# Kernel optimization log

Measured on AMD Instinct MI355X. Metric: run time of the kernel, lower is better.

Reference implementation:

```python
import jax, jax.numpy as jnp
import numpy as np

B, S, D, H = 2, 2048, 1024, 16
HD = D // H  # head_dim = 64
ROPE_BASE = 10000.0
NEG = -1e9


def rope_cos_sin(seq_len, head_dim, dtype):
    inv_freq = 1.0 / (ROPE_BASE ** (jnp.arange(0, head_dim, 2, dtype=jnp.float32) / head_dim))
    t = jnp.arange(seq_len, dtype=jnp.float32)
    freqs = jnp.outer(t, inv_freq)              # [S, HD/2]
    emb = jnp.concatenate([freqs, freqs], axis=-1)  # [S, HD]
    return jnp.cos(emb).astype(dtype), jnp.sin(emb).astype(dtype)


def rotate_half(x):
    half = x.shape[-1] // 2
    return jnp.concatenate([-x[..., half:], x[..., :half]], axis=-1)


def setup_inputs() -> dict:
    key = jax.random.key(0)
    ks = jax.random.split(key, 9)
    s = 0.02
    x = jax.random.normal(ks[0], (B, S, D), dtype=jnp.float32)
    # additive causal mask: 0 on/below diagonal, -1e9 above
    mask = jnp.where(jnp.tril(jnp.ones((S, S), dtype=bool)), 0.0, NEG).astype(jnp.float32)
    params = {
        'Wq': jax.random.normal(ks[1], (D, D), jnp.float32) * s,
        'bq': jnp.zeros((D,), jnp.float32),
        'Wk': jax.random.normal(ks[2], (D, D), jnp.float32) * s,
        'bk': jnp.zeros((D,), jnp.float32),
        'Wv': jax.random.normal(ks[3], (D, D), jnp.float32) * s,
        'bv': jnp.zeros((D,), jnp.float32),
        'Wo': jax.random.normal(ks[4], (D, D), jnp.float32) * s,
        'bo': jnp.zeros((D,), jnp.float32),
    }
    return {'x': x, 'mask': mask, **params}


def reference(x, mask, Wq, bq, Wk, bk, Wv, bv, Wo, bo):
    Bv, Sv, Dv = x.shape
    q = (x @ Wq + bq).reshape(Bv, Sv, H, HD).transpose(0, 2, 1, 3)  # [B,H,S,HD]
    k = (x @ Wk + bk).reshape(Bv, Sv, H, HD).transpose(0, 2, 1, 3)
    v = (x @ Wv + bv).reshape(Bv, Sv, H, HD).transpose(0, 2, 1, 3)
    cos, sin = rope_cos_sin(Sv, HD, x.dtype)      # [S, HD]
    cos = cos[None, None]                          # [1,1,S,HD]
    sin = sin[None, None]
    q = q * cos + rotate_half(q) * sin
    k = k * cos + rotate_half(k) * sin
    scale = jnp.asarray(np.sqrt(HD), x.dtype)
    scores = jnp.einsum('bhqd,bhkd->bhqk', q, k) / scale  # [B,H,S,S]
    scores = scores + mask[None, None]
    attn = jax.nn.softmax(scores, axis=-1)
    out = jnp.einsum('bhqk,bhkd->bhqd', attn, v)   # [B,H,S,HD]
    out = out.transpose(0, 2, 1, 3).reshape(Bv, Sv, Dv)
    return out @ Wo + bo
```

## Files before the change

### kernel.cpp

```cpp
#include <hip/hip_runtime.h>
#include <hip/hip_bf16.h>
#include <cstdint>

typedef __bf16 bf16;
typedef __bf16 bf16x4 __attribute__((ext_vector_type(4)));
typedef __bf16 bf16x8 __attribute__((ext_vector_type(8)));
typedef float f32x4 __attribute__((ext_vector_type(4)));

#define DEV __device__ __forceinline__

DEV void gl_lds16(const void* g, void* l) {
    __builtin_amdgcn_global_load_lds(
        (__attribute__((address_space(1))) void*)(uintptr_t)g,
        (__attribute__((address_space(3))) void*)(uint32_t)(uintptr_t)l,
        16, 0, 0);
}

DEV f32x4 mfma16(bf16x8 a, bf16x8 b, f32x4 c) {
    return __builtin_amdgcn_mfma_f32_16x16x32_bf16(a, b, c, 0, 0, 0);
}

__global__ __launch_bounds__(256) void prep_k(
    const float* __restrict__ x, bf16* __restrict__ xb,
    const float* __restrict__ w0, const float* __restrict__ w1,
    const float* __restrict__ w2, const float* __restrict__ w3,
    bf16* __restrict__ WT, float* __restrict__ cosT, float* __restrict__ sinT) {
    __shared__ float t[32][33];
    const int blk = (int)blockIdx.x;
    const int tid = threadIdx.x;
    if (blk < 4096) {
        const int i = blk * 256 + tid;
        const float4 v = ((const float4*)x)[i];
        bf16x4 o = {(bf16)v.x, (bf16)v.y, (bf16)v.z, (bf16)v.w};
        *(bf16x4*)(xb + (size_t)i * 4) = o;
    } else if (blk < 8192) {
        const int j = blk - 4096;
        const int z = j >> 10, jy = (j >> 5) & 31, jx = j & 31;
        const float* W = z == 0 ? w0 : z == 1 ? w1 : z == 2 ? w2 : w3;
        bf16* dst = WT + (size_t)z * 1024 * 1024;
        const int tx = tid & 31, ty = tid >> 5;
        const int kb = jx * 32, nb = jy * 32;
#pragma unroll
        for (int i = 0; i < 4; ++i)
            t[ty + i * 8][tx] = W[(size_t)(kb + ty + i * 8) * 1024 + nb + tx];
        __syncthreads();
#pragma unroll
        for (int i = 0; i < 4; ++i)
            dst[(size_t)(nb + ty + i * 8) * 1024 + kb + tx] = (bf16)t[tx][ty + i * 8];
    } else {
        const int tt = (blk - 8192) * 256 + tid;
        const int s = tt >> 6, i = tt & 31;
        const float inv = expf(-(float)i * (9.210340371976184f / 32.0f));
        const float ang = (float)s * inv;
        cosT[tt] = cosf(ang);
        sinT[tt] = sinf(ang);
    }
}

__global__ __launch_bounds__(512, 1) void gemm256_k(
    const bf16* __restrict__ A, const bf16* __restrict__ BT,
    const float* __restrict__ bq, const float* __restrict__ bk,
    const float* __restrict__ bv,
    bf16* __restrict__ outQ, bf16* __restrict__ outK, bf16* __restrict__ outV,
    const float* __restrict__ cosT, const float* __restrict__ sinT) {
    extern __shared__ char smem[];
    const int tid = threadIdx.x;
    const int lane = tid & 63, wv = tid >> 6;
    const int wm2 = wv >> 2, wn2 = wv & 3;
    const int q = lane & 15, g = lane >> 4;

    const int gid = (int)blockIdx.x;
    const int xcd = gid & 7, idx = gid >> 3;
    const int bm = (xcd & 3) * 4 + (idx & 3);
    const int bn = (xcd >> 2) * 6 + (idx >> 2);

    const bf16* Ab = A + (size_t)bm * 256 * 1024;
    const bf16* Bb = BT + (size_t)bn * 256 * 1024;

    auto stage = [&](int b, int kb) {
        char* base = smem + b * 65536;
#pragma unroll
        for (int i = 0; i < 4; ++i) {
            const int Xs = i * 8192 + tid * 16;
            const int row = Xs >> 7;
            const int cb = (Xs & 127) ^ ((row & 7) << 4);
            gl_lds16(Ab + (size_t)row * 1024 + kb + (cb >> 1), base + Xs);
        }
#pragma unroll
        for (int i = 0; i < 4; ++i) {
            const int Xs = i * 8192 + tid * 16;
            const int row = Xs >> 7;
            const int cb = (Xs & 127) ^ ((row & 7) << 4);
            gl_lds16(Bb + (size_t)row * 1024 + kb + (cb >> 1), base + 32768 + Xs);
        }
    };

    f32x4 acc[8][4] = {};

    stage(0, 0);

    for (int t = 0; t < 16; ++t) {
        asm volatile("s_waitcnt vmcnt(0)" ::: "memory");
        __builtin_amdgcn_s_barrier();
        if (t + 1 < 16) stage((t + 1) & 1, (t + 1) * 64);
        const char* cbuf = smem + (t & 1) * 65536;
        bf16x8 bfr[4];
#pragma unroll
        for (int p = 0; p < 4; ++p) {
            const int ks = p >> 1, mih = p & 1;
            if (mih == 0) {
#pragma unroll
                for (int ni = 0; ni < 4; ++ni) {
                    const int row = wn2 * 64 + ni * 16 + q;
                    bfr[ni] = *(const bf16x8*)(cbuf + 32768 + row * 128 +
                                               ((ks * 64 + g * 16) ^ ((q & 7) << 4)));
                }
            }
            bf16x8 af[4];
#pragma unroll
            for (int j = 0; j < 4; ++j) {
                const int row = wm2 * 128 + (mih * 4 + j) * 16 + q;
                af[j] = *(const bf16x8*)(cbuf + row * 128 +
                                         ((ks * 64 + g * 16) ^ ((q & 7) << 4)));
            }
            __builtin_amdgcn_s_setprio(1);
#pragma unroll
            for (int j = 0; j < 4; ++j)
#pragma unroll
                for (int ni = 0; ni < 4; ++ni)
                    acc[mih * 4 + j][ni] = mfma16(af[j], bfr[ni], acc[mih * 4 + j][ni]);
            __builtin_amdgcn_s_setprio(0);
        }
    }

    const int n0 = bn * 256 + wn2 * 64;
    const int seg = n0 >> 10;
    const int nloc = n0 & 1023;
    const int h = nloc >> 6;
    const float* bias = seg == 0 ? bq : (seg == 1 ? bk : bv);
    const float qsc = (seg == 0) ? 0.125f : 1.0f;
    float bvv[4];
#pragma unroll
    for (int ni = 0; ni < 4; ++ni) bvv[ni] = bias[nloc + ni * 16 + q];

    if (seg < 2) {
        bf16* dst = seg == 0 ? outQ : outK;
#pragma unroll
        for (int mi = 0; mi < 8; ++mi) {
#pragma unroll
            for (int r = 0; r < 4; ++r) {
                const int m = bm * 256 + wm2 * 128 + mi * 16 + g * 4 + r;
                const int s = m & 2047, bb = m >> 11;
                const size_t rowb = ((size_t)((bb << 4) | h) * 2048 + s) * 64;
#pragma unroll
                for (int ni = 0; ni < 4; ++ni) {
                    const int hd = ni * 16 + q;
                    const float c = cosT[s * 64 + hd], sn = sinT[s * 64 + hd];
                    const float v0 = acc[mi][ni][r] + bvv[ni];
                    const float v1 = acc[mi][ni ^ 2][r] + bvv[ni ^ 2];
                    dst[rowb + hd] = (bf16)((v0 * c + (ni < 2 ? -v1 : v1) * sn) * qsc);
                }
            }
        }
    } else {
        __builtin_amdgcn_s_barrier();
        bf16* Tw = (bf16*)smem + wv * (64 * 72);
        const int bb = (bm * 256) >> 11;
        bf16* vbase = outV + (size_t)((bb << 4) | h) * (64 * 2048);
#pragma unroll
        for (int sh = 0; sh < 2; ++sh) {
#pragma unroll
            for (int mi2 = 0; mi2 < 4; ++mi2)
#pragma unroll
                for (int ni = 0; ni < 4; ++ni)
#pragma unroll
                    for (int r = 0; r < 4; ++r)
                        Tw[(ni * 16 + q) * 72 + mi2 * 16 + g * 4 + r] =
                            (bf16)(acc[sh * 4 + mi2][ni][r] + bvv[ni]);
            const int s0 = ((bm * 256) & 2047) + wm2 * 128 + sh * 64;
#pragma unroll
            for (int i = 0; i < 8; ++i) {
                const int row = i * 8 + (lane >> 3);
                const int col = (lane & 7) * 8;
                bf16x8 vvv = *(const bf16x8*)(Tw + row * 72 + col);
                *(bf16x8*)(vbase + (size_t)row * 2048 + s0 + col) = vvv;
            }
        }
    }
}

__global__ __launch_bounds__(256) void gemmo_k(
    const bf16* __restrict__ A, const bf16* __restrict__ BT,
    const float* __restrict__ bias0, float* __restrict__ outF) {
    extern __shared__ char smem[];
    const int tid = threadIdx.x;
    const int lane = tid & 63;
    const int wv = tid >> 6;
    const int wm = wv >> 1, wn = wv & 1;
    const int bm = blockIdx.x, bn = blockIdx.y;
    const int q = lane & 15, g = lane >> 4;

    const bf16* Ab = A + (size_t)bm * 128 * 1024;
    const bf16* Bb = BT + (size_t)bn * 128 * 1024;
    const int r0 = tid >> 2, c0 = (tid & 3) * 8;

    auto stage = [&](int b, int kb) {
        char* base = smem + b * 16384;
        gl_lds16(Ab + (size_t)r0 * 1024 + kb + c0, base + tid * 16);
        gl_lds16(Ab + (size_t)(r0 + 64) * 1024 + kb + c0, base + 4096 + tid * 16);
        gl_lds16(Bb + (size_t)r0 * 1024 + kb + c0, base + 8192 + tid * 16);
        gl_lds16(Bb + (size_t)(r0 + 64) * 1024 + kb + c0, base + 12288 + tid * 16);
    };

    f32x4 acc[4][4] = {};

    stage(0, 0);
    stage(1, 32);
    asm volatile("s_waitcnt vmcnt(4)" ::: "memory");
    __builtin_amdgcn_s_barrier();

    for (int kt = 0; kt < 32; ++kt) {
        if (kt + 2 < 32) stage((kt + 2) % 3, (kt + 2) * 32);
        const bf16* As = (const bf16*)(smem + (kt % 3) * 16384);
        const bf16* Bs = As + 128 * 32;
        bf16x8 af[4], bfr[4];
#pragma unroll
        for (int mi = 0; mi < 4; ++mi)
            af[mi] = *(const bf16x8*)(As + (wm * 64 + mi * 16 + q) * 32 + g * 8);
#pragma unroll
        for (int ni = 0; ni < 4; ++ni)
            bfr[ni] = *(const bf16x8*)(Bs + (wn * 64 + ni * 16 + q) * 32 + g * 8);
#pragma unroll
        for (int mi = 0; mi < 4; ++mi)
#pragma unroll
            for (int ni = 0; ni < 4; ++ni)
                acc[mi][ni] = mfma16(af[mi], bfr[ni], acc[mi][ni]);
        if (kt + 2 < 32) asm volatile("s_waitcnt vmcnt(4)" ::: "memory");
        else             asm volatile("s_waitcnt vmcnt(0)" ::: "memory");
        __builtin_amdgcn_s_barrier();
    }

    const int n0 = bn * 128 + wn * 64;
    float bvv[4];
#pragma unroll
    for (int ni = 0; ni < 4; ++ni) bvv[ni] = bias0[n0 + ni * 16 + q];
#pragma unroll
    for (int mi = 0; mi < 4; ++mi)
#pragma unroll
        for (int r = 0; r < 4; ++r) {
            const int m = bm * 128 + wm * 64 + mi * 16 + g * 4 + r;
#pragma unroll
            for (int ni = 0; ni < 4; ++ni)
                outF[(size_t)m * 1024 + n0 + ni * 16 + q] = acc[mi][ni][r] + bvv[ni];
        }
}

__global__ __launch_bounds__(512, 2) void attn_k(const bf16* __restrict__ Qr,
                                                 const bf16* __restrict__ Kr,
                                                 const bf16* __restrict__ Vt,
                                                 bf16* __restrict__ AO) {
    const int gid = (int)blockIdx.x;
    const int xcd = gid & 7;
    const int bh = xcd + 8 * ((gid >> 3) & 3);
    const int idx = gid >> 5;
    const int p = idx >> 1;
    const int h = 1 - (idx & 1);
    const int tid = threadIdx.x;
    const int lane = tid & 63, wv = tid >> 6;
    const int q = lane & 15, g = lane >> 4;
    const int qt_w = (wv >> 2) ? p : (15 - p);
    const int q0w = qt_w * 128 + h * 64 + (wv & 3) * 16;
    const int nt = 31 - 2 * p + h;
    const size_t hb = (size_t)bh * (2048 * 64);
    extern __shared__ char smem[];
    bf16* P = (bf16*)(smem + 49152 + wv * 2304);

    const bf16* Kg = Kr + hb;
    const bf16* Vg = Vt + hb;
    const int swz = (q & 7) << 4;

    auto stage = [&](int b, int kb) {
        char* base = smem + b * 16384;
        {
            const int X = tid * 16;
            const int row = X >> 7;
            const int cbg = (X & 127) ^ ((row & 7) << 4);
            gl_lds16(Kg + (size_t)(kb + row) * 64 + (cbg >> 1), base + X);
        }
        {
            const int X = tid * 16;
            const int row = X >> 7;
            const int cbg = (X & 127) ^ ((row & 7) << 4);
            gl_lds16(Vg + (size_t)row * 2048 + kb + (cbg >> 1), base + 8192 + X);
        }
    };

    bf16x8 qf[2];
    {
        const bf16* qp = Qr + hb + (size_t)(q0w + q) * 64 + g * 8;
        qf[0] = *(const bf16x8*)(qp);
        qf[1] = *(const bf16x8*)(qp + 32);
    }
    f32x4 o[4] = {};
    float l_run = 0.0f;
    const f32x4 z4 = {0.f, 0.f, 0.f, 0.f};
    const int rmax = q0w + 15;

    stage(0, 0);
    stage(1, 64);
    asm volatile("s_waitcnt vmcnt(2)" ::: "memory");
    __builtin_amdgcn_s_barrier();

    for (int kt = 0; kt < nt; ++kt) {
        const int kb = kt * 64;
        if (kt + 2 < nt) stage((kt + 2) % 3, kb + 128);
        if (kb <= rmax) {
            char* Kl = smem + (kt % 3) * 16384;
            char* Vl = Kl + 8192;
            f32x4 st[4];
            __builtin_amdgcn_s_setprio(1);
#pragma unroll
            for (int f = 0; f < 4; ++f) {
                const int row = f * 16 + q;
                const bf16x8 k0 = *(const bf16x8*)(Kl + row * 128 + ((g * 16) ^ swz));
                const bf16x8 k1 = *(const bf16x8*)(Kl + row * 128 + ((64 + g * 16) ^ swz));
                f32x4 t0 = mfma16(k0, qf[0], z4);
                st[f] = mfma16(k1, qf[1], t0);
            }
            __builtin_amdgcn_s_setprio(0);
            bf16x8 vf[4][2];
#pragma unroll
            for (int nf = 0; nf < 4; ++nf) {
                const int row = nf * 16 + q;
                vf[nf][0] = *(const bf16x8*)(Vl + row * 128 + ((g * 16) ^ swz));
                vf[nf][1] = *(const bf16x8*)(Vl + row * 128 + ((64 + g * 16) ^ swz));
            }
            float tsum = 0.f;
            if (kb + 63 > q0w) {
#pragma unroll
                for (int f = 0; f < 4; ++f)
#pragma unroll
                    for (int r = 0; r < 4; ++r) {
                        float sv = st[f][r];
                        if (kb + f * 16 + g * 4 + r > q0w + q) sv = -3.0e38f;
                        const float pv = __expf(sv);
                        st[f][r] = pv;
                        tsum += pv;
                    }
            } else {
#pragma unroll
                for (int f = 0; f < 4; ++f)
#pragma unroll
                    for (int r = 0; r < 4; ++r) {
                        const float pv = __expf(st[f][r]);
                        st[f][r] = pv;
                        tsum += pv;
                    }
            }
            l_run += tsum;
#pragma unroll
            for (int f = 0; f < 4; ++f) {
                bf16x4 pv = {(bf16)st[f][0], (bf16)st[f][1],
                             (bf16)st[f][2], (bf16)st[f][3]};
                *(bf16x4*)&P[q * 72 + f * 16 + g * 4] = pv;
            }
            __builtin_amdgcn_s_setprio(1);
#pragma unroll
            for (int t = 0; t < 2; ++t) {
                const bf16x8 pa = *(const bf16x8*)&P[q * 72 + t * 32 + g * 8];
#pragma unroll
                for (int nf = 0; nf < 4; ++nf)
                    o[nf] = mfma16(pa, vf[nf][t], o[nf]);
            }
            __builtin_amdgcn_s_setprio(0);
        }
        if (kt + 2 < nt) asm volatile("s_waitcnt vmcnt(2)" ::: "memory");
        else             asm volatile("s_waitcnt vmcnt(0)" ::: "memory");
        __builtin_amdgcn_s_barrier();
    }

    l_run += __shfl_xor(l_run, 16);
    l_run += __shfl_xor(l_run, 32);
    float li[4];
#pragma unroll
    for (int r = 0; r < 4; ++r) li[r] = 1.0f / __shfl(l_run, g * 4 + r);
    const int b_ = bh >> 4, h_ = bh & 15;
#pragma unroll
    for (int nf = 0; nf < 4; ++nf)
#pragma unroll
        for (int r = 0; r < 4; ++r) {
            const int qg = q0w + g * 4 + r;
            AO[(size_t)(b_ * 2048 + qg) * 1024 + h_ * 64 + nf * 16 + q] =
                (bf16)(o[nf][r] * li[r]);
        }
}


extern "C" void kernel_launch(void* const* d_in, const int* in_sizes, int n_in,
                              void* d_out, int out_size, void* d_ws, size_t ws_size,
                              hipStream_t stream) {
    const float* x  = (const float*)d_in[0];
    const float* Wq = (const float*)d_in[2];
    const float* bq = (const float*)d_in[3];
    const float* Wk = (const float*)d_in[4];
    const float* bk = (const float*)d_in[5];
    const float* Wv = (const float*)d_in[6];
    const float* bv = (const float*)d_in[7];
    const float* Wo = (const float*)d_in[8];
    const float* bo = (const float*)d_in[9];
    float* out = (float*)d_out;
    char* ws = (char*)d_ws;
    const size_t MB_ = 1024 * 1024;
    bf16* xb    = (bf16*)(ws);
    bf16* WT    = (bf16*)(ws + 8 * MB_);
    bf16* Qrp   = (bf16*)(ws + 16 * MB_);
    bf16* Krp   = (bf16*)(ws + 24 * MB_);
    bf16* Vt    = (bf16*)(ws + 32 * MB_);
    bf16* AO    = (bf16*)(ws + 40 * MB_);
    float* cosT = (float*)(ws + 48 * MB_);
    float* sinT = (float*)(ws + 48 * MB_ + 512 * 1024);

    hipFuncSetAttribute((const void*)gemm256_k,
                        hipFuncAttributeMaxDynamicSharedMemorySize, 131072);

    prep_k<<<8704, 256, 0, stream>>>(x, xb, Wq, Wk, Wv, Wo, WT, cosT, sinT);
    gemm256_k<<<dim3(192), 512, 131072, stream>>>(xb, WT, bq, bk, bv,
                                                  Qrp, Krp, Vt, cosT, sinT);
    attn_k<<<dim3(512, 1), 512, 67584, stream>>>(Qrp, Krp, Vt, AO);
    gemmo_k<<<dim3(32, 8), 256, 49152, stream>>>(AO, WT + (size_t)3072 * 1024, bo, out);
}
```

Baseline: 95.69 us.

## Shrink QKV GEMM tile to 128x256 with BK=32 for higher occupancy

The fused QKV projection GEMM moves from 256x256 tiles with a 64-wide K step and 128KB of LDS to 128x256 tiles with a 32-wide K step and 48KB of LDS. The grid doubles to 384 blocks and the launch bounds allow several blocks per CU, so more blocks are in flight to hide load latency and the tail is smaller. The V-transpose epilogue is serialized into two rounds of four waves to fit the smaller LDS. The cost is less data reuse per tile, twice as many barrier-synchronized K iterations, and a new LDS swizzle pattern.

```diff
diff --git a/kernel.cpp b/kernel.cpp
--- a/kernel.cpp
+++ b/kernel.cpp
@@ -57,7 +57,7 @@
     }
 }
 
-__global__ __launch_bounds__(512, 1) void gemm256_k(
+__global__ __launch_bounds__(512, 4) void gemm256_k(
     const bf16* __restrict__ A, const bf16* __restrict__ BT,
     const float* __restrict__ bq, const float* __restrict__ bk,
     const float* __restrict__ bv,
@@ -71,66 +71,57 @@
 
     const int gid = (int)blockIdx.x;
     const int xcd = gid & 7, idx = gid >> 3;
-    const int bm = (xcd & 3) * 4 + (idx & 3);
-    const int bn = (xcd >> 2) * 6 + (idx >> 2);
-
-    const bf16* Ab = A + (size_t)bm * 256 * 1024;
+    const int bm = (xcd & 3) * 8 + (idx & 7);
+    const int bn = (xcd >> 2) * 6 + (idx >> 3);
+
+    const bf16* Ab = A + (size_t)bm * 128 * 1024;
     const bf16* Bb = BT + (size_t)bn * 256 * 1024;
 
     auto stage = [&](int b, int kb) {
-        char* base = smem + b * 65536;
-#pragma unroll
-        for (int i = 0; i < 4; ++i) {
+        char* base = smem + b * 24576;
+        {
+            const int Xs = tid * 16;
+            const int row = Xs >> 6;
+            const int cb = (Xs & 63) ^ ((row & 3) << 4);
+            gl_lds16(Ab + (size_t)row * 1024 + kb + (cb >> 1), base + Xs);
+        }
+#pragma unroll
+        for (int i = 0; i < 2; ++i) {
             const int Xs = i * 8192 + tid * 16;
-            const int row = Xs >> 7;
-            const int cb = (Xs & 127) ^ ((row & 7) << 4);
-            gl_lds16(Ab + (size_t)row * 1024 + kb + (cb >> 1), base + Xs);
-        }
-#pragma unroll
-        for (int i = 0; i < 4; ++i) {
-            const int Xs = i * 8192 + tid * 16;
-            const int row = Xs >> 7;
-            const int cb = (Xs & 127) ^ ((row & 7) << 4);
-            gl_lds16(Bb + (size_t)row * 1024 + kb + (cb >> 1), base + 32768 + Xs);
+            const int row = Xs >> 6;
+            const int cb = (Xs & 63) ^ ((row & 3) << 4);
+            gl_lds16(Bb + (size_t)row * 1024 + kb + (cb >> 1), base + 8192 + Xs);
         }
     };
 
-    f32x4 acc[8][4] = {};
+    f32x4 acc[4][4] = {};
+    const int swz = (q & 3) << 4;
 
     stage(0, 0);
 
-    for (int t = 0; t < 16; ++t) {
+    for (int t = 0; t < 32; ++t) {
         asm volatile("s_waitcnt vmcnt(0)" ::: "memory");
         __builtin_amdgcn_s_barrier();
-        if (t + 1 < 16) stage((t + 1) & 1, (t + 1) * 64);
-        const char* cbuf = smem + (t & 1) * 65536;
-        bf16x8 bfr[4];
-#pragma unroll
-        for (int p = 0; p < 4; ++p) {
-            const int ks = p >> 1, mih = p & 1;
-            if (mih == 0) {
-#pragma unroll
-                for (int ni = 0; ni < 4; ++ni) {
-                    const int row = wn2 * 64 + ni * 16 + q;
-                    bfr[ni] = *(const bf16x8*)(cbuf + 32768 + row * 128 +
-                                               ((ks * 64 + g * 16) ^ ((q & 7) << 4)));
-                }
-            }
-            bf16x8 af[4];
-#pragma unroll
-            for (int j = 0; j < 4; ++j) {
-                const int row = wm2 * 128 + (mih * 4 + j) * 16 + q;
-                af[j] = *(const bf16x8*)(cbuf + row * 128 +
-                                         ((ks * 64 + g * 16) ^ ((q & 7) << 4)));
-            }
-            __builtin_amdgcn_s_setprio(1);
-#pragma unroll
-            for (int j = 0; j < 4; ++j)
-#pragma unroll
-                for (int ni = 0; ni < 4; ++ni)
-                    acc[mih * 4 + j][ni] = mfma16(af[j], bfr[ni], acc[mih * 4 + j][ni]);
-            __builtin_amdgcn_s_setprio(0);
-        }
+        if (t + 1 < 32) stage((t + 1) & 1, (t + 1) * 32);
+        const char* cbuf = smem + (t & 1) * 24576;
+        bf16x8 af[4], bfr[4];
+#pragma unroll
+        for (int ni = 0; ni < 4; ++ni) {
+            const int row = wn2 * 64 + ni * 16 + q;
+            bfr[ni] = *(const bf16x8*)(cbuf + 8192 + row * 64 + ((g * 16) ^ swz));
+        }
+#pragma unroll
+        for (int j = 0; j < 4; ++j) {
+            const int row = wm2 * 64 + j * 16 + q;
+            af[j] = *(const bf16x8*)(cbuf + row * 64 + ((g * 16) ^ swz));
+        }
+        __builtin_amdgcn_s_setprio(1);
+#pragma unroll
+        for (int j = 0; j < 4; ++j)
+#pragma unroll
+            for (int ni = 0; ni < 4; ++ni)
+                acc[j][ni] = mfma16(af[j], bfr[ni], acc[j][ni]);
+        __builtin_amdgcn_s_setprio(0);
     }
 
     const int n0 = bn * 256 + wn2 * 64;
@@ -146,10 +137,10 @@
     if (seg < 2) {
         bf16* dst = seg == 0 ? outQ : outK;
 #pragma unroll
-        for (int mi = 0; mi < 8; ++mi) {
+        for (int mi = 0; mi < 4; ++mi) {
 #pragma unroll
             for (int r = 0; r < 4; ++r) {
-                const int m = bm * 256 + wm2 * 128 + mi * 16 + g * 4 + r;
+                const int m = bm * 128 + wm2 * 64 + mi * 16 + g * 4 + r;
                 const int s = m & 2047, bb = m >> 11;
                 const size_t rowb = ((size_t)((bb << 4) | h) * 2048 + s) * 64;
 #pragma unroll
@@ -163,27 +154,29 @@
             }
         }
     } else {
-        __builtin_amdgcn_s_barrier();
-        bf16* Tw = (bf16*)smem + wv * (64 * 72);
-        const int bb = (bm * 256) >> 11;
+        const int bb = (bm * 128) >> 11;
         bf16* vbase = outV + (size_t)((bb << 4) | h) * (64 * 2048);
-#pragma unroll
-        for (int sh = 0; sh < 2; ++sh) {
-#pragma unroll
-            for (int mi2 = 0; mi2 < 4; ++mi2)
-#pragma unroll
-                for (int ni = 0; ni < 4; ++ni)
-#pragma unroll
-                    for (int r = 0; r < 4; ++r)
-                        Tw[(ni * 16 + q) * 72 + mi2 * 16 + g * 4 + r] =
-                            (bf16)(acc[sh * 4 + mi2][ni][r] + bvv[ni]);
-            const int s0 = ((bm * 256) & 2047) + wm2 * 128 + sh * 64;
-#pragma unroll
-            for (int i = 0; i < 8; ++i) {
-                const int row = i * 8 + (lane >> 3);
-                const int col = (lane & 7) * 8;
-                bf16x8 vvv = *(const bf16x8*)(Tw + row * 72 + col);
-                *(bf16x8*)(vbase + (size_t)row * 2048 + s0 + col) = vvv;
+        const int s0 = ((bm * 128) & 2047) + wm2 * 64;
+#pragma unroll
+        for (int rnd = 0; rnd < 2; ++rnd) {
+            __builtin_amdgcn_s_barrier();
+            if ((wv >> 2) == rnd) {
+                bf16* Tw = (bf16*)smem + (wv & 3) * (64 * 72);
+#pragma unroll
+                for (int mi2 = 0; mi2 < 4; ++mi2)
+#pragma unroll
+                    for (int ni = 0; ni < 4; ++ni)
+#pragma unroll
+                        for (int r = 0; r < 4; ++r)
+                            Tw[(ni * 16 + q) * 72 + mi2 * 16 + g * 4 + r] =
+                                (bf16)(acc[mi2][ni][r] + bvv[ni]);
+#pragma unroll
+                for (int i = 0; i < 8; ++i) {
+                    const int row = i * 8 + (lane >> 3);
+                    const int col = (lane & 7) * 8;
+                    bf16x8 vvv = *(const bf16x8*)(Tw + row * 72 + col);
+                    *(bf16x8*)(vbase + (size_t)row * 2048 + s0 + col) = vvv;
+                }
             }
         }
     }
@@ -420,12 +413,9 @@
     float* cosT = (float*)(ws + 48 * MB_);
     float* sinT = (float*)(ws + 48 * MB_ + 512 * 1024);
 
-    hipFuncSetAttribute((const void*)gemm256_k,
-                        hipFuncAttributeMaxDynamicSharedMemorySize, 131072);
-
     prep_k<<<8704, 256, 0, stream>>>(x, xb, Wq, Wk, Wv, Wo, WT, cosT, sinT);
-    gemm256_k<<<dim3(192), 512, 131072, stream>>>(xb, WT, bq, bk, bv,
-                                                  Qrp, Krp, Vt, cosT, sinT);
+    gemm256_k<<<dim3(384), 512, 49152, stream>>>(xb, WT, bq, bk, bv,
+                                                 Qrp, Krp, Vt, cosT, sinT);
     attn_k<<<dim3(512, 1), 512, 67584, stream>>>(Qrp, Krp, Vt, AO);
     gemmo_k<<<dim3(32, 8), 256, 49152, stream>>>(AO, WT + (size_t)3072 * 1024, bo, out);
 }
```

Result: no change. 95.83 us (+0.1%).
